# Optimization experiments

Hardware: AMD Instinct MI355X
Metric: run time of the kernel (lower is better)

Reference implementation:

```python
import jax, jax.numpy as jnp
import numpy as np
from jax import lax

B, T, I, H, L, C = 128, 784, 1, 256, 20, 10  # batch, seq_len, input, hidden, layers, classes


def setup_inputs() -> dict:
    key = jax.random.key(0)
    ks = jax.random.split(key, 9)
    s = 1.0 / np.sqrt(H)  # torch nn.RNN init: U(-1/sqrt(H), 1/sqrt(H))
    u = lambda k, shape: jax.random.uniform(k, shape, jnp.float32, -s, s)
    return {
        "x": jax.random.normal(ks[0], (B, T, I), jnp.float32),
        "W_ih0": u(ks[1], (H, I)),        # layer 0 input proj
        "b_ih0": u(ks[2], (H,)),
        "W_ih": u(ks[3], (L - 1, H, H)),  # layers 1..L-1 input proj
        "b_ih": u(ks[4], (L - 1, H)),
        "W_hh": u(ks[5], (L, H, H)),      # recurrent weights, all layers
        "b_hh": u(ks[6], (L, H)),
        "W_fc": u(ks[7], (C, H)),         # classification head
        "b_fc": u(ks[8], (C,)),
    }


def _rnn_layer(x_seq, W_ih, b_ih, W_hh, b_hh):
    """One vanilla relu-RNN layer. x_seq: [B,T,in] -> [B,T,H]."""
    # Hoist the input projection out of the scan (batched GEMM over all timesteps).
    xp = jnp.einsum('bti,hi->bth', x_seq, W_ih) + b_ih  # [B,T,H]
    h0 = jnp.zeros((x_seq.shape[0], W_hh.shape[0]), x_seq.dtype)

    def step(h, xt):
        h = jax.nn.relu(xt + h @ W_hh.T + b_hh)
        return h, h

    _, ys = lax.scan(step, h0, jnp.swapaxes(xp, 0, 1))  # scan over time
    return jnp.swapaxes(ys, 0, 1)  # [B,T,H]


def reference(x, W_ih0, b_ih0, W_ih, b_ih, W_hh, b_hh, W_fc, b_fc):
    h = _rnn_layer(x, W_ih0, b_ih0, W_hh[0], b_hh[0])
    for l in range(L - 1):  # fixed small layer loop
        h = _rnn_layer(h, W_ih[l], b_ih[l], W_hh[l + 1], b_hh[l + 1])
    last_hidden = h[:, -1, :]  # [B,H]
    return last_hidden @ W_fc.T + b_fc  # [B,C]
```

## Files before the change

kernel.cpp:

```cpp
#include <hip/hip_runtime.h>
#include <hip/hip_fp16.h>


#define B_    128
#define T_    784
#define H_    256
#define L_    20
#define C_    10
#define G_    8
#define BM_   16
#define S_    4
#define NS_   196
#define SW_   280
#define RQWS_ 4096
#define TPB_  512

typedef _Float16 v8h __attribute__((ext_vector_type(8)));
typedef _Float16 v4h __attribute__((ext_vector_type(4)));
typedef float    v4f __attribute__((ext_vector_type(4)));
typedef unsigned long long u64;

union U64H { u64 u; _Float16 h[4]; };

__device__ __forceinline__ void bar_lds() {
    asm volatile("s_waitcnt lgkmcnt(0)" ::: "memory");
    __builtin_amdgcn_s_barrier();
    asm volatile("" ::: "memory");
}
__device__ __forceinline__ void bar_full() {
    asm volatile("s_waitcnt vmcnt(0) lgkmcnt(0)" ::: "memory");
    __builtin_amdgcn_s_barrier();
    asm volatile("" ::: "memory");
}

__global__ __launch_bounds__(TPB_, 2)
void rnn_wavefront(const float* __restrict__ x,
                   const float* __restrict__ W_ih0,
                   const float* __restrict__ b_ih0,
                   const float* __restrict__ W_ih,
                   const float* __restrict__ b_ih,
                   const float* __restrict__ W_hh,
                   const float* __restrict__ b_hh,
                   const float* __restrict__ W_fc,
                   const float* __restrict__ b_fc,
                   float* __restrict__ out,
                   unsigned* __restrict__ prod,
                   unsigned* __restrict__ cons,
                   u64* __restrict__ ring,
                   int rmask)
{
    const int l    = blockIdx.x >> 3;
    const int g    = blockIdx.x & 7;
    const int tid  = threadIdx.x;
    const int lane = tid & 63;
    const int wave = tid >> 6;
    const int quad = lane >> 4;
    const int s16  = lane & 15;
    const int nbase = wave * 32;
    const int m_e  = tid >> 5;
    const int n_e  = (tid & 31) * 8;

    __shared__ __align__(16) _Float16 bufX[S_][BM_][SW_];
    __shared__ __align__(16) _Float16 lH[2][BM_][SW_];

    for (int i = tid; i < 2 * BM_ * SW_; i += TPB_) (&lH[0][0][0])[i] = (_Float16)0.f;

    v8h wf[16][2];
#pragma unroll
    for (int kt = 0; kt < 16; ++kt) {
        const int k0 = kt * 32 + quad * 8;
#pragma unroll
        for (int nt = 0; nt < 2; ++nt) {
            const int j = nbase + nt * 16 + s16;
            v8h w;
            if (kt < 8) {
                if (l == 0) {
#pragma unroll
                    for (int i = 0; i < 8; ++i) w[i] = (_Float16)0.f;
                } else {
                    const float* src = &W_ih[(((size_t)(l - 1) * H_) + j) * H_ + k0];
#pragma unroll
                    for (int i = 0; i < 8; ++i) w[i] = (_Float16)src[i];
                }
            } else {
                const float* src = &W_hh[(((size_t)l * H_) + j) * H_ + (k0 - 256)];
#pragma unroll
                for (int i = 0; i < 8; ++i) w[i] = (_Float16)src[i];
            }
            wf[kt][nt] = w;
        }
    }

    float bias[2][4], w0v[2][4];
#pragma unroll
    for (int nt = 0; nt < 2; ++nt)
#pragma unroll
        for (int r = 0; r < 4; ++r) {
            const int j = nbase + nt * 16 + quad * 4 + r;
            bias[nt][r] = b_hh[l * H_ + j] + ((l == 0) ? b_ih0[j] : b_ih[(l - 1) * H_ + j]);
            w0v[nt][r]  = (l == 0) ? W_ih0[j] : 0.f;
        }

    unsigned* upprod = prod + ((l > 0 ? l - 1 : 0) * G_ + g);
    unsigned* myprod = prod + (l * G_ + g);
    unsigned* mycons = cons + (l * G_ + g);
    unsigned* dncons = cons + (((l < L_ - 1) ? l + 1 : l) * G_ + g);
    const unsigned R = (unsigned)rmask + 1u;
    u64* myring = ring + ((size_t)(l * G_ + g) * (size_t)R) * RQWS_;
    u64* upring = ring + ((size_t)((l > 0 ? l - 1 : 0) * G_ + g) * (size_t)R) * RQWS_;

    unsigned pSeen = 0, cSeen = 0;
    const size_t eidx = (size_t)m_e * 64 + (size_t)(tid & 31) * 2;

    if (l > 0) {
        if (tid == 64) {
            while (pSeen < 2u) {
                pSeen = __hip_atomic_load(upprod, __ATOMIC_RELAXED,
                                          __HIP_MEMORY_SCOPE_AGENT);
                if (pSeen < 2u) __builtin_amdgcn_s_sleep(2);
            }
        }
        __syncthreads();
#pragma unroll
        for (int jj = 0; jj < S_; ++jj) {
            u64 v0 = __hip_atomic_load(upring + (size_t)jj * 1024 + eidx,
                                       __ATOMIC_RELAXED, __HIP_MEMORY_SCOPE_AGENT);
            u64 v1 = __hip_atomic_load(upring + (size_t)jj * 1024 + eidx + 1,
                                       __ATOMIC_RELAXED, __HIP_MEMORY_SCOPE_AGENT);
            *(u64*)&bufX[jj][m_e][n_e]     = v0;
            *(u64*)&bufX[jj][m_e][n_e + 4] = v1;
        }
    }

    for (int s = 0; s < NS_; ++s) {
        const bool pfOK = (l > 0) && (s + 1 < NS_);
        u64 pfv[S_][2];
        v4h XPh[S_][2];

#pragma unroll
        for (int j = 0; j < S_; ++j) {
            const int t = S_ * s + j;
            if (j == 1) bar_full(); else bar_lds();

            if (j == 0) {
                if (tid == 0 && l > 0)
                    __hip_atomic_store(mycons, (unsigned)(s + 1), __ATOMIC_RELAXED,
                                       __HIP_MEMORY_SCOPE_AGENT);
                if (tid == 64 && pfOK) {
                    const unsigned tgt = (unsigned)(s + 2);
                    while (pSeen < tgt) {
                        pSeen = __hip_atomic_load(upprod, __ATOMIC_RELAXED,
                                                  __HIP_MEMORY_SCOPE_AGENT);
                        if (pSeen < tgt) __builtin_amdgcn_s_sleep(2);
                    }
                }
                if (tid == 128 && l < L_ - 1 && s >= (int)R) {
                    const unsigned tgt = (unsigned)(s - (int)R + 1);
                    while (cSeen < tgt) {
                        cSeen = __hip_atomic_load(dncons, __ATOMIC_RELAXED,
                                                  __HIP_MEMORY_SCOPE_AGENT);
                        if (cSeen < tgt) __builtin_amdgcn_s_sleep(2);
                    }
                }

                if (l > 0) {
                    v4f xpa[S_][2];
#pragma unroll
                    for (int jj = 0; jj < S_; ++jj)
#pragma unroll
                        for (int nt = 0; nt < 2; ++nt)
                            xpa[jj][nt] = (v4f){bias[nt][0], bias[nt][1],
                                                bias[nt][2], bias[nt][3]};
#pragma unroll
                    for (int jj = 0; jj < S_; ++jj) {
#pragma unroll
                        for (int kt = 0; kt < 8; ++kt) {
                            v8h a = *(const v8h*)&bufX[jj][s16][kt * 32 + quad * 8];
                            xpa[jj][0] = __builtin_amdgcn_mfma_f32_16x16x32_f16(wf[kt][0], a, xpa[jj][0], 0, 0, 0);
                            xpa[jj][1] = __builtin_amdgcn_mfma_f32_16x16x32_f16(wf[kt][1], a, xpa[jj][1], 0, 0, 0);
                        }
                    }
#pragma unroll
                    for (int jj = 0; jj < S_; ++jj)
#pragma unroll
                        for (int nt = 0; nt < 2; ++nt)
#pragma unroll
                            for (int r = 0; r < 4; ++r)
                                XPh[jj][nt][r] = (_Float16)xpa[jj][nt][r];
                } else {
#pragma unroll
                    for (int jj = 0; jj < S_; ++jj) {
                        const float xv = x[(size_t)(g * BM_ + s16) * T_ + (S_ * s + jj)];
#pragma unroll
                        for (int nt = 0; nt < 2; ++nt)
#pragma unroll
                            for (int r = 0; r < 4; ++r)
                                XPh[jj][nt][r] = (_Float16)(bias[nt][r] + xv * w0v[nt][r]);
                    }
                }
            }

            if (j == 1) {
                if (tid == 0 && l < L_ - 1 && s >= 1)
                    __hip_atomic_store(myprod, (unsigned)s, __ATOMIC_RELAXED,
                                       __HIP_MEMORY_SCOPE_AGENT);
                if (pfOK) {
                    const u64* base = upring + (size_t)((s + 1) & rmask) * RQWS_;
#pragma unroll
                    for (int jj = 0; jj < S_; ++jj) {
                        pfv[jj][0] = __hip_atomic_load(base + (size_t)jj * 1024 + eidx,
                                                       __ATOMIC_RELAXED,
                                                       __HIP_MEMORY_SCOPE_AGENT);
                        pfv[jj][1] = __hip_atomic_load(base + (size_t)jj * 1024 + eidx + 1,
                                                       __ATOMIC_RELAXED,
                                                       __HIP_MEMORY_SCOPE_AGENT);
                    }
                }
            }

            if (l < L_ - 1 && t > 0) {
                u64 e0 = *(const u64*)&lH[t & 1][m_e][n_e];
                u64 e1 = *(const u64*)&lH[t & 1][m_e][n_e + 4];
                u64* d = myring + (size_t)(((t - 1) >> 2) & rmask) * RQWS_
                                + (size_t)((t - 1) & 3) * 1024 + eidx;
                __hip_atomic_store(d,     e0, __ATOMIC_RELAXED, __HIP_MEMORY_SCOPE_AGENT);
                __hip_atomic_store(d + 1, e1, __ATOMIC_RELAXED, __HIP_MEMORY_SCOPE_AGENT);
            }

            v4f acc0 = (v4f){0.f, 0.f, 0.f, 0.f};
            v4f acc1 = (v4f){0.f, 0.f, 0.f, 0.f};
#pragma unroll
            for (int kt = 8; kt < 16; ++kt) {
                v8h a = *(const v8h*)&lH[t & 1][s16][(kt - 8) * 32 + quad * 8];
                acc0 = __builtin_amdgcn_mfma_f32_16x16x32_f16(wf[kt][0], a, acc0, 0, 0, 0);
                acc1 = __builtin_amdgcn_mfma_f32_16x16x32_f16(wf[kt][1], a, acc1, 0, 0, 0);
            }

#pragma unroll
            for (int nt = 0; nt < 2; ++nt) {
                const v4f av = nt ? acc1 : acc0;
                U64H pk;
#pragma unroll
                for (int r = 0; r < 4; ++r) {
                    float v = (float)XPh[j][nt][r] + av[r];
                    v = fmaxf(v, 0.f);
                    pk.h[r] = (_Float16)v;
                }
                *(u64*)&lH[(t + 1) & 1][s16][nbase + nt * 16 + quad * 4] = pk.u;
            }

            if (j == S_ - 1) {
                bar_lds();
                if (pfOK) {
#pragma unroll
                    for (int jj = 0; jj < S_; ++jj) {
                        *(u64*)&bufX[jj][m_e][n_e]     = pfv[jj][0];
                        *(u64*)&bufX[jj][m_e][n_e + 4] = pfv[jj][1];
                    }
                }
            }
        }
    }

    if (l < L_ - 1) {
        u64 e0 = *(const u64*)&lH[0][m_e][n_e];
        u64 e1 = *(const u64*)&lH[0][m_e][n_e + 4];
        u64* d = myring + (size_t)(((T_ - 1) >> 2) & rmask) * RQWS_
                        + (size_t)3 * 1024 + eidx;
        __hip_atomic_store(d,     e0, __ATOMIC_RELAXED, __HIP_MEMORY_SCOPE_AGENT);
        __hip_atomic_store(d + 1, e1, __ATOMIC_RELAXED, __HIP_MEMORY_SCOPE_AGENT);
        __syncthreads();
        if (tid == 0)
            __hip_atomic_store(myprod, (unsigned)NS_, __ATOMIC_RELAXED,
                               __HIP_MEMORY_SCOPE_AGENT);
    } else {
        __syncthreads();
        if (tid < BM_ * C_) {
            const int bl = tid / C_;
            const int c  = tid % C_;
            float sum = b_fc[c];
            for (int k = 0; k < H_; ++k) sum += (float)lH[0][bl][k] * W_fc[c * H_ + k];
            out[(size_t)(g * BM_ + bl) * C_ + c] = sum;
        }
    }
}

extern "C" void kernel_launch(void* const* d_in, const int* in_sizes, int n_in,
                              void* d_out, int out_size, void* d_ws, size_t ws_size,
                              hipStream_t stream) {
    const float* x     = (const float*)d_in[0];
    const float* W_ih0 = (const float*)d_in[1];
    const float* b_ih0 = (const float*)d_in[2];
    const float* W_ih  = (const float*)d_in[3];
    const float* b_ih  = (const float*)d_in[4];
    const float* W_hh  = (const float*)d_in[5];
    const float* b_hh  = (const float*)d_in[6];
    const float* W_fc  = (const float*)d_in[7];
    const float* b_fc  = (const float*)d_in[8];
    float* out = (float*)d_out;

    const size_t cntBytes = (size_t)L_ * G_ * sizeof(unsigned);
    unsigned* prod = (unsigned*)d_ws;
    unsigned* cons = (unsigned*)((char*)d_ws + cntBytes);
    u64* ring      = (u64*)((char*)d_ws + 2 * cntBytes);

    const size_t slotBytes = (size_t)RQWS_ * 8;
    const size_t base = 2 * cntBytes;
    int R = 4;
    if (ws_size >= base + (size_t)L_ * G_ * 16 * slotBytes) R = 16;
    else if (ws_size >= base + (size_t)L_ * G_ * 8 * slotBytes) R = 8;

    hipMemsetAsync(d_ws, 0, 2 * cntBytes, stream);

    rnn_wavefront<<<dim3(L_ * G_), dim3(TPB_), 0, stream>>>(
        x, W_ih0, b_ih0, W_ih, b_ih, W_hh, b_hh, W_fc, b_fc,
        out, prod, cons, ring, R - 1);
}
```

Baseline: 1.131 ms.

## Split waves into recurrent and input-projection groups with one-chunk lookahead

```diff
diff --git a/kernel.cpp b/kernel.cpp
--- a/kernel.cpp
+++ b/kernel.cpp
@@ -12,8 +12,11 @@
 #define S_    4
 #define NS_   196
 #define SW_   280
+#define XSW_  260
 #define RQWS_ 4096
 #define TPB_  512
+#define HW_   4
+#define NT_   4
 
 typedef _Float16 v8h __attribute__((ext_vector_type(8)));
 typedef _Float16 v4h __attribute__((ext_vector_type(4)));
@@ -54,52 +57,56 @@
     const int tid  = threadIdx.x;
     const int lane = tid & 63;
     const int wave = tid >> 6;
+    const bool hwv = wave < HW_;
+    const int wsub = hwv ? wave : wave - HW_;
     const int quad = lane >> 4;
     const int s16  = lane & 15;
-    const int nbase = wave * 32;
+    const int nbase = wsub * 64;
     const int m_e  = tid >> 5;
     const int n_e  = (tid & 31) * 8;
 
-    __shared__ __align__(16) _Float16 bufX[S_][BM_][SW_];
+    __shared__ __align__(16) _Float16 bufX[2][S_][BM_][SW_];
     __shared__ __align__(16) _Float16 lH[2][BM_][SW_];
+    __shared__ __align__(16) _Float16 xps[2][S_][BM_][XSW_];
 
     for (int i = tid; i < 2 * BM_ * SW_; i += TPB_) (&lH[0][0][0])[i] = (_Float16)0.f;
 
-    v8h wf[16][2];
-#pragma unroll
-    for (int kt = 0; kt < 16; ++kt) {
+    v8h wf[8][NT_];
+#pragma unroll
+    for (int kt = 0; kt < 8; ++kt) {
         const int k0 = kt * 32 + quad * 8;
 #pragma unroll
-        for (int nt = 0; nt < 2; ++nt) {
+        for (int nt = 0; nt < NT_; ++nt) {
             const int j = nbase + nt * 16 + s16;
             v8h w;
-            if (kt < 8) {
-                if (l == 0) {
-#pragma unroll
-                    for (int i = 0; i < 8; ++i) w[i] = (_Float16)0.f;
-                } else {
-                    const float* src = &W_ih[(((size_t)(l - 1) * H_) + j) * H_ + k0];
-#pragma unroll
-                    for (int i = 0; i < 8; ++i) w[i] = (_Float16)src[i];
-                }
+            if (hwv) {
+                const float* src = &W_hh[(((size_t)l * H_) + j) * H_ + k0];
+#pragma unroll
+                for (int i = 0; i < 8; ++i) w[i] = (_Float16)src[i];
+            } else if (l > 0) {
+                const float* src = &W_ih[(((size_t)(l - 1) * H_) + j) * H_ + k0];
+#pragma unroll
+                for (int i = 0; i < 8; ++i) w[i] = (_Float16)src[i];
             } else {
-                const float* src = &W_hh[(((size_t)l * H_) + j) * H_ + (k0 - 256)];
-#pragma unroll
-                for (int i = 0; i < 8; ++i) w[i] = (_Float16)src[i];
+#pragma unroll
+                for (int i = 0; i < 8; ++i) w[i] = (_Float16)0.f;
             }
             wf[kt][nt] = w;
         }
     }
 
-    float bias[2][4], w0v[2][4];
-#pragma unroll
-    for (int nt = 0; nt < 2; ++nt)
-#pragma unroll
-        for (int r = 0; r < 4; ++r) {
-            const int j = nbase + nt * 16 + quad * 4 + r;
-            bias[nt][r] = b_hh[l * H_ + j] + ((l == 0) ? b_ih0[j] : b_ih[(l - 1) * H_ + j]);
-            w0v[nt][r]  = (l == 0) ? W_ih0[j] : 0.f;
-        }
+    float bias[NT_][4], w0v[NT_][4];
+    if (!hwv) {
+#pragma unroll
+        for (int nt = 0; nt < NT_; ++nt)
+#pragma unroll
+            for (int r = 0; r < 4; ++r) {
+                const int j = nbase + nt * 16 + quad * 4 + r;
+                bias[nt][r] = b_hh[l * H_ + j] +
+                              ((l == 0) ? b_ih0[j] : b_ih[(l - 1) * H_ + j]);
+                w0v[nt][r]  = (l == 0) ? W_ih0[j] : 0.f;
+            }
+    }
 
     unsigned* upprod = prod + ((l > 0 ? l - 1 : 0) * G_ + g);
     unsigned* myprod = prod + (l * G_ + g);
@@ -122,20 +129,57 @@
         }
         __syncthreads();
 #pragma unroll
+        for (int sl = 0; sl < 2; ++sl)
+#pragma unroll
+            for (int jj = 0; jj < S_; ++jj) {
+                u64 v0 = __hip_atomic_load(upring + (size_t)sl * RQWS_ + (size_t)jj * 1024 + eidx,
+                                           __ATOMIC_RELAXED, __HIP_MEMORY_SCOPE_AGENT);
+                u64 v1 = __hip_atomic_load(upring + (size_t)sl * RQWS_ + (size_t)jj * 1024 + eidx + 1,
+                                           __ATOMIC_RELAXED, __HIP_MEMORY_SCOPE_AGENT);
+                *(u64*)&bufX[sl][jj][m_e][n_e]     = v0;
+                *(u64*)&bufX[sl][jj][m_e][n_e + 4] = v1;
+            }
+        __syncthreads();
+    }
+    if (!hwv) {
+#pragma unroll
         for (int jj = 0; jj < S_; ++jj) {
-            u64 v0 = __hip_atomic_load(upring + (size_t)jj * 1024 + eidx,
-                                       __ATOMIC_RELAXED, __HIP_MEMORY_SCOPE_AGENT);
-            u64 v1 = __hip_atomic_load(upring + (size_t)jj * 1024 + eidx + 1,
-                                       __ATOMIC_RELAXED, __HIP_MEMORY_SCOPE_AGENT);
-            *(u64*)&bufX[jj][m_e][n_e]     = v0;
-            *(u64*)&bufX[jj][m_e][n_e + 4] = v1;
-        }
-    }
+            v4f xpa[NT_];
+#pragma unroll
+            for (int nt = 0; nt < NT_; ++nt)
+                xpa[nt] = (v4f){bias[nt][0], bias[nt][1], bias[nt][2], bias[nt][3]};
+            if (l > 0) {
+#pragma unroll
+                for (int kt = 0; kt < 8; ++kt) {
+                    v8h a = *(const v8h*)&bufX[0][jj][s16][kt * 32 + quad * 8];
+#pragma unroll
+                    for (int nt = 0; nt < NT_; ++nt)
+                        xpa[nt] = __builtin_amdgcn_mfma_f32_16x16x32_f16(
+                                      wf[kt][nt], a, xpa[nt], 0, 0, 0);
+                }
+            } else {
+                const float xv = x[(size_t)(g * BM_ + s16) * T_ + jj];
+#pragma unroll
+                for (int nt = 0; nt < NT_; ++nt)
+#pragma unroll
+                    for (int r = 0; r < 4; ++r)
+                        xpa[nt][r] = bias[nt][r] + xv * w0v[nt][r];
+            }
+#pragma unroll
+            for (int nt = 0; nt < NT_; ++nt) {
+                U64H pk;
+#pragma unroll
+                for (int r = 0; r < 4; ++r) pk.h[r] = (_Float16)xpa[nt][r];
+                *(u64*)&xps[0][jj][s16][nbase + nt * 16 + quad * 4] = pk.u;
+            }
+        }
+    }
+    __syncthreads();
 
     for (int s = 0; s < NS_; ++s) {
-        const bool pfOK = (l > 0) && (s + 1 < NS_);
+        const bool stOK = (l > 0) && (s + 2 < NS_);
+        const bool xOK  = (s + 1 < NS_);
         u64 pfv[S_][2];
-        v4h XPh[S_][2];
 
 #pragma unroll
         for (int j = 0; j < S_; ++j) {
@@ -143,11 +187,13 @@
             if (j == 1) bar_full(); else bar_lds();
 
             if (j == 0) {
-                if (tid == 0 && l > 0)
-                    __hip_atomic_store(mycons, (unsigned)(s + 1), __ATOMIC_RELAXED,
+                if (tid == 0 && l > 0) {
+                    const unsigned cv = (unsigned)((s + 2 <= NS_) ? s + 2 : NS_);
+                    __hip_atomic_store(mycons, cv, __ATOMIC_RELAXED,
                                        __HIP_MEMORY_SCOPE_AGENT);
-                if (tid == 64 && pfOK) {
-                    const unsigned tgt = (unsigned)(s + 2);
+                }
+                if (tid == 64 && stOK) {
+                    const unsigned tgt = (unsigned)(s + 3);
                     while (pSeen < tgt) {
                         pSeen = __hip_atomic_load(upprod, __ATOMIC_RELAXED,
                                                   __HIP_MEMORY_SCOPE_AGENT);
@@ -162,50 +208,14 @@
                         if (cSeen < tgt) __builtin_amdgcn_s_sleep(2);
                     }
                 }
-
-                if (l > 0) {
-                    v4f xpa[S_][2];
-#pragma unroll
-                    for (int jj = 0; jj < S_; ++jj)
-#pragma unroll
-                        for (int nt = 0; nt < 2; ++nt)
-                            xpa[jj][nt] = (v4f){bias[nt][0], bias[nt][1],
-                                                bias[nt][2], bias[nt][3]};
-#pragma unroll
-                    for (int jj = 0; jj < S_; ++jj) {
-#pragma unroll
-                        for (int kt = 0; kt < 8; ++kt) {
-                            v8h a = *(const v8h*)&bufX[jj][s16][kt * 32 + quad * 8];
-                            xpa[jj][0] = __builtin_amdgcn_mfma_f32_16x16x32_f16(wf[kt][0], a, xpa[jj][0], 0, 0, 0);
-                            xpa[jj][1] = __builtin_amdgcn_mfma_f32_16x16x32_f16(wf[kt][1], a, xpa[jj][1], 0, 0, 0);
-                        }
-                    }
-#pragma unroll
-                    for (int jj = 0; jj < S_; ++jj)
-#pragma unroll
-                        for (int nt = 0; nt < 2; ++nt)
-#pragma unroll
-                            for (int r = 0; r < 4; ++r)
-                                XPh[jj][nt][r] = (_Float16)xpa[jj][nt][r];
-                } else {
-#pragma unroll
-                    for (int jj = 0; jj < S_; ++jj) {
-                        const float xv = x[(size_t)(g * BM_ + s16) * T_ + (S_ * s + jj)];
-#pragma unroll
-                        for (int nt = 0; nt < 2; ++nt)
-#pragma unroll
-                            for (int r = 0; r < 4; ++r)
-                                XPh[jj][nt][r] = (_Float16)(bias[nt][r] + xv * w0v[nt][r]);
-                    }
-                }
             }
 
             if (j == 1) {
                 if (tid == 0 && l < L_ - 1 && s >= 1)
                     __hip_atomic_store(myprod, (unsigned)s, __ATOMIC_RELAXED,
                                        __HIP_MEMORY_SCOPE_AGENT);
-                if (pfOK) {
-                    const u64* base = upring + (size_t)((s + 1) & rmask) * RQWS_;
+                if (stOK) {
+                    const u64* base = upring + (size_t)((s + 2) & rmask) * RQWS_;
 #pragma unroll
                     for (int jj = 0; jj < S_; ++jj) {
                         pfv[jj][0] = __hip_atomic_load(base + (size_t)jj * 1024 + eidx,
@@ -227,36 +237,70 @@
                 __hip_atomic_store(d + 1, e1, __ATOMIC_RELAXED, __HIP_MEMORY_SCOPE_AGENT);
             }
 
-            v4f acc0 = (v4f){0.f, 0.f, 0.f, 0.f};
-            v4f acc1 = (v4f){0.f, 0.f, 0.f, 0.f};
-#pragma unroll
-            for (int kt = 8; kt < 16; ++kt) {
-                v8h a = *(const v8h*)&lH[t & 1][s16][(kt - 8) * 32 + quad * 8];
-                acc0 = __builtin_amdgcn_mfma_f32_16x16x32_f16(wf[kt][0], a, acc0, 0, 0, 0);
-                acc1 = __builtin_amdgcn_mfma_f32_16x16x32_f16(wf[kt][1], a, acc1, 0, 0, 0);
-            }
-
-#pragma unroll
-            for (int nt = 0; nt < 2; ++nt) {
-                const v4f av = nt ? acc1 : acc0;
-                U64H pk;
-#pragma unroll
-                for (int r = 0; r < 4; ++r) {
-                    float v = (float)XPh[j][nt][r] + av[r];
-                    v = fmaxf(v, 0.f);
-                    pk.h[r] = (_Float16)v;
-                }
-                *(u64*)&lH[(t + 1) & 1][s16][nbase + nt * 16 + quad * 4] = pk.u;
-            }
-
-            if (j == S_ - 1) {
-                bar_lds();
-                if (pfOK) {
-#pragma unroll
-                    for (int jj = 0; jj < S_; ++jj) {
-                        *(u64*)&bufX[jj][m_e][n_e]     = pfv[jj][0];
-                        *(u64*)&bufX[jj][m_e][n_e + 4] = pfv[jj][1];
-                    }
+            if (hwv) {
+                v4h xph[NT_];
+#pragma unroll
+                for (int nt = 0; nt < NT_; ++nt)
+                    xph[nt] = *(const v4h*)&xps[s & 1][j][s16][nbase + nt * 16 + quad * 4];
+
+                v4f acc[NT_];
+#pragma unroll
+                for (int nt = 0; nt < NT_; ++nt) acc[nt] = (v4f){0.f, 0.f, 0.f, 0.f};
+#pragma unroll
+                for (int kt = 0; kt < 8; ++kt) {
+                    v8h a = *(const v8h*)&lH[t & 1][s16][kt * 32 + quad * 8];
+#pragma unroll
+                    for (int nt = 0; nt < NT_; ++nt)
+                        acc[nt] = __builtin_amdgcn_mfma_f32_16x16x32_f16(
+                                      wf[kt][nt], a, acc[nt], 0, 0, 0);
+                }
+#pragma unroll
+                for (int nt = 0; nt < NT_; ++nt) {
+                    U64H pk;
+#pragma unroll
+                    for (int r = 0; r < 4; ++r) {
+                        float v = (float)xph[nt][r] + acc[nt][r];
+                        v = fmaxf(v, 0.f);
+                        pk.h[r] = (_Float16)v;
+                    }
+                    *(u64*)&lH[(t + 1) & 1][s16][nbase + nt * 16 + quad * 4] = pk.u;
+                }
+            } else if (xOK) {
+                v4f xpa[NT_];
+#pragma unroll
+                for (int nt = 0; nt < NT_; ++nt)
+                    xpa[nt] = (v4f){bias[nt][0], bias[nt][1], bias[nt][2], bias[nt][3]};
+                if (l > 0) {
+#pragma unroll
+                    for (int kt = 0; kt < 8; ++kt) {
+                        v8h a = *(const v8h*)&bufX[(s + 1) & 1][j][s16][kt * 32 + quad * 8];
+#pragma unroll
+                        for (int nt = 0; nt < NT_; ++nt)
+                            xpa[nt] = __builtin_amdgcn_mfma_f32_16x16x32_f16(
+                                          wf[kt][nt], a, xpa[nt], 0, 0, 0);
+                    }
+                } else {
+                    const float xv = x[(size_t)(g * BM_ + s16) * T_ + (S_ * (s + 1) + j)];
+#pragma unroll
+                    for (int nt = 0; nt < NT_; ++nt)
+#pragma unroll
+                        for (int r = 0; r < 4; ++r)
+                            xpa[nt][r] = bias[nt][r] + xv * w0v[nt][r];
+                }
+#pragma unroll
+                for (int nt = 0; nt < NT_; ++nt) {
+                    U64H pk;
+#pragma unroll
+                    for (int r = 0; r < 4; ++r) pk.h[r] = (_Float16)xpa[nt][r];
+                    *(u64*)&xps[(s + 1) & 1][j][s16][nbase + nt * 16 + quad * 4] = pk.u;
+                }
+            }
+
+            if (j == S_ - 1 && stOK) {
+#pragma unroll
+                for (int jj = 0; jj < S_; ++jj) {
+                    *(u64*)&bufX[s & 1][jj][m_e][n_e]     = pfv[jj][0];
+                    *(u64*)&bufX[s & 1][jj][m_e][n_e + 4] = pfv[jj][1];
                 }
             }
         }
```

New measurement: 1.127 ms. No clear change (-0.3%).
